# Performance work log

Hardware: AMD Instinct MI355X
Metric: run time of the kernel (lower is better)

## Reference

```python
import jax, jax.numpy as jnp
import numpy as np

WS = 7            # window size
NH = 6            # num heads
HD = 32           # head dim
DISP = WS // 2    # cyclic shift displacement (shifted=True)
SCALE = HD ** -0.5


def _create_mask(ws, d, upper_lower, left_right):
    m = np.zeros((ws * ws, ws * ws), np.float32)
    if upper_lower:
        m[-d * ws:, :-d * ws] = -np.inf
        m[:-d * ws, -d * ws:] = -np.inf
    if left_right:
        m = m.reshape(ws, ws, ws, ws)
        m[:, -d:, :, :-d] = -np.inf
        m[:, :-d, :, -d:] = -np.inf
        m = m.reshape(ws * ws, ws * ws)
    return m


def _relative_indices(ws):
    idx = np.array([[x, y] for x in range(ws) for y in range(ws)])
    return idx[None, :, :] - idx[:, None, :] + ws - 1  # (ws^2, ws^2, 2)


_REL = _relative_indices(WS)
_UL_MASK = _create_mask(WS, DISP, True, False)
_LR_MASK = _create_mask(WS, DISP, False, True)


def setup_inputs() -> dict:
    key = jax.random.key(0)
    ks = jax.random.split(key, 5)
    B, H, W, C = 32, 56, 56, 192
    inner = NH * HD
    return {
        "x": jax.random.normal(ks[0], (B, H, W, C), jnp.float32),
        "w_qkv": jax.random.normal(ks[1], (3 * inner, C), jnp.float32) * 0.02,
        "pos_embedding": jax.random.normal(ks[2], (2 * WS - 1, 2 * WS - 1), jnp.float32),
        "w_out": jax.random.normal(ks[3], (C, inner), jnp.float32) * 0.02,
        "b_out": jax.random.normal(ks[4], (C,), jnp.float32) * 0.02,
    }


def reference(x, w_qkv, pos_embedding, w_out, b_out):
    B, H, W, C = x.shape
    nwh, nww = H // WS, W // WS
    n = WS * WS
    nw = nwh * nww

    # cyclic shift
    x = jnp.roll(x, shift=(-DISP, -DISP), axis=(1, 2))

    qkv = x @ w_qkv.T  # (B,H,W,3*inner)

    def to_windows(t):
        # (B,H,W,inner) -> (B, NH, nw, n, HD)
        t = t.reshape(B, nwh, WS, nww, WS, NH, HD)
        t = t.transpose(0, 5, 1, 3, 2, 4, 6)
        return t.reshape(B, NH, nw, n, HD)

    q, k, v = map(to_windows, jnp.split(qkv, 3, axis=-1))

    dots = jnp.einsum('bhwid,bhwjd->bhwij', q, k) * SCALE

    # gathered relative-position bias
    bias = pos_embedding[_REL[:, :, 0], _REL[:, :, 1]]  # (n, n)
    dots = dots + bias

    # shift masks (static per-window additive mask)
    mask_full = np.zeros((nw, n, n), np.float32)
    mask_full[-nww:] += _UL_MASK
    mask_full[nww - 1::nww] += _LR_MASK
    dots = dots + jnp.asarray(mask_full)[None, None]

    attn = jax.nn.softmax(dots, axis=-1)
    out = jnp.einsum('bhwij,bhwjd->bhwid', attn, v)

    # windows back to image layout
    out = out.reshape(B, NH, nwh, nww, WS, WS, HD)
    out = out.transpose(0, 2, 4, 3, 5, 1, 6).reshape(B, H, W, NH * HD)

    out = out @ w_out.T + b_out
    return jnp.roll(out, shift=(DISP, DISP), axis=(1, 2))
```

## Files before the change

### kernel.cpp

```cpp
#include <hip/hip_runtime.h>
#include <hip/hip_bf16.h>

#define PIX 3136
#define MTOT 100352
#define SCALE 0.17677669529663687f

typedef __attribute__((ext_vector_type(8))) short bf16x8;
typedef __attribute__((ext_vector_type(4))) float f32x4;
typedef __attribute__((ext_vector_type(8))) unsigned short u16x8;

__device__ __forceinline__ unsigned short f2bf(float f) {
    __hip_bfloat16 h = __float2bfloat16(f);
    return *reinterpret_cast<unsigned short*>(&h);
}

__device__ __forceinline__ u16x8 packbf(float4 a, float4 b) {
    u16x8 r;
    r[0] = f2bf(a.x); r[1] = f2bf(a.y); r[2] = f2bf(a.z); r[3] = f2bf(a.w);
    r[4] = f2bf(b.x); r[5] = f2bf(b.y); r[6] = f2bf(b.z); r[7] = f2bf(b.w);
    return r;
}

__global__ __launch_bounds__(256) void qkv_mfma(
        const float* __restrict__ x, const float* __restrict__ wqkv,
        unsigned short* __restrict__ qo, unsigned short* __restrict__ ko,
        unsigned short* __restrict__ vo) {
    __shared__ __align__(16) unsigned char Al[128 * 384];
    __shared__ __align__(16) unsigned char Bl[64 * 384];
    const int tid = threadIdx.x;
    const int lane = tid & 63, wid = tid >> 6;
    const int G = lane >> 4, l16 = lane & 15;
    const int row0 = blockIdx.x * 128;

    {
        const int r = tid >> 1, half = tid & 1;
        const int gr = row0 + r;
        const int b = gr / PIX;
        const int rem = gr - b * PIX;
        const int w = rem / 49;
        const int i = rem - w * 49;
        const int yi = (i * 9363) >> 16;
        const int xi = i - yi * 7;
        int sh = (w >> 3) * 7 + yi + 3; if (sh >= 56) sh -= 56;
        int sw = (w & 7) * 7 + xi + 3; if (sw >= 56) sw -= 56;
        const float* src = x + ((size_t)(b * 56 + sh) * 56 + sw) * 192 + half * 96;
        const int swz = (r & 7) << 4;
#pragma unroll
        for (int c = 0; c < 12; c++) {
            float4 f0 = *(const float4*)(src + c * 8);
            float4 f1 = *(const float4*)(src + c * 8 + 4);
            const int off = half * 192 + c * 16;
            *(u16x8*)&Al[r * 384 + (off ^ swz)] = packbf(f0, f1);
        }
    }

    const int wr = wid >> 1, wc = wid & 1;
    f32x4 acc[4][2];
#pragma unroll
    for (int a = 0; a < 4; a++)
#pragma unroll
        for (int bb = 0; bb < 2; bb++) acc[a][bb] = (f32x4){0.f, 0.f, 0.f, 0.f};
    bf16x8 areg[4][6];

    for (int nt = 0; nt < 9; nt++) {
        __syncthreads();
        {
            const int rB = tid >> 2, q4 = tid & 3;
            const float* src = wqkv + (size_t)(nt * 64 + rB) * 192 + q4 * 48;
            const int swz = (rB & 7) << 4;
#pragma unroll
            for (int c = 0; c < 6; c++) {
                float4 f0 = *(const float4*)(src + c * 8);
                float4 f1 = *(const float4*)(src + c * 8 + 4);
                const int off = q4 * 96 + c * 16;
                *(u16x8*)&Bl[rB * 384 + (off ^ swz)] = packbf(f0, f1);
            }
        }
        __syncthreads();
        if (nt == 0) {
#pragma unroll
            for (int mi = 0; mi < 4; mi++) {
                const int rr = wr * 64 + mi * 16 + l16;
                const int swz = (rr & 7) << 4;
#pragma unroll
                for (int ks = 0; ks < 6; ks++)
                    areg[mi][ks] = *(const bf16x8*)&Al[rr * 384 + ((ks * 64 + G * 16) ^ swz)];
            }
        }
#pragma unroll
        for (int ks = 0; ks < 6; ks++) {
#pragma unroll
            for (int ni = 0; ni < 2; ni++) {
                const int rb = wc * 32 + ni * 16 + l16;
                bf16x8 bf = *(const bf16x8*)&Bl[rb * 384 + ((ks * 64 + G * 16) ^ ((rb & 7) << 4))];
#pragma unroll
                for (int mi = 0; mi < 4; mi++)
                    acc[mi][ni] = __builtin_amdgcn_mfma_f32_16x16x32_bf16(
                        areg[mi][ks], bf, acc[mi][ni], 0, 0, 0);
            }
        }
#pragma unroll
        for (int mi = 0; mi < 4; mi++) {
#pragma unroll
            for (int ni = 0; ni < 2; ni++) {
                const int nb = nt * 64 + wc * 32 + ni * 16;
                const int part = nb / 192;
                const int nn = nb - part * 192;
                const int head = nn >> 5;
                const int d = (nn & 31) + l16;
                unsigned short* dst = part == 0 ? qo : part == 1 ? ko : vo;
#pragma unroll
                for (int r = 0; r < 4; r++) {
                    const int rm = row0 + wr * 64 + mi * 16 + G * 4 + r;
                    const int b2 = rm / PIX;
                    const int rem2 = rm - b2 * PIX;
                    dst[((size_t)(b2 * 6 + head) * PIX + rem2) * 32 + d] = f2bf(acc[mi][ni][r]);
                    acc[mi][ni][r] = 0.f;
                }
            }
        }
    }
}

__global__ __launch_bounds__(256) void attn_mfma(
        const unsigned short* __restrict__ qg, const unsigned short* __restrict__ kg,
        const unsigned short* __restrict__ vg, const float* __restrict__ pe,
        unsigned short* __restrict__ ao) {
    __shared__ float pes[169];
    __shared__ __align__(16) unsigned char Pl[4][8192];
    __shared__ __align__(16) unsigned char Vl[4][4096];
    const int tid = threadIdx.x, lane = tid & 63, wid = tid >> 6;
    const int G = lane >> 4, l16 = lane & 15;
    if (tid < 169) pes[tid] = pe[tid];

    const int gw = blockIdx.x * 4 + wid;
    const int b = gw / 384;
    const int r384 = gw - b * 384;
    const int head = r384 >> 6;
    const int w = r384 & 63;
    const int wh = w >> 3, ww = w & 7;

#pragma unroll
    for (int z = 0; z < 4; z++)
        *(f32x4*)&Vl[wid][z * 1024 + lane * 16] = (f32x4){0.f, 0.f, 0.f, 0.f};

    const size_t base = ((size_t)(b * 6 + head) * PIX + w * 49) * 32;
    const unsigned short* qb = qg + base;
    const unsigned short* kb = kg + base;
    const unsigned short* vb = vg + base;

    for (int t = lane; t < 196; t += 64) {
        const int j = t >> 2, d0 = (t & 3) * 8;
        u16x8 vv = *(const u16x8*)(vb + j * 32 + d0);
#pragma unroll
        for (int e = 0; e < 8; e++) {
            const int d = d0 + e;
            *(unsigned short*)&Vl[wid][d * 128 + ((j * 2) ^ ((d & 7) << 4))] = vv[e];
        }
    }

    bf16x8 qf[4], kf[4];
    const bf16x8 zf = {0, 0, 0, 0, 0, 0, 0, 0};
#pragma unroll
    for (int mi = 0; mi < 4; mi++) {
        const int rr = mi * 16 + l16;
        qf[mi] = (rr < 49) ? *(const bf16x8*)(qb + rr * 32 + G * 8) : zf;
        kf[mi] = (rr < 49) ? *(const bf16x8*)(kb + rr * 32 + G * 8) : zf;
    }
    __syncthreads();

    const f32x4 zc = (f32x4){0.f, 0.f, 0.f, 0.f};
    f32x4 s[4][4];
#pragma unroll
    for (int mi = 0; mi < 4; mi++)
#pragma unroll
        for (int nj = 0; nj < 4; nj++)
            s[mi][nj] = __builtin_amdgcn_mfma_f32_16x16x32_bf16(qf[mi], kf[nj], zc, 0, 0, 0);

    const bool ulm = (wh == 7), lrm = (ww == 7);
    int jv[4], yj[4], xj[4];
#pragma unroll
    for (int nj = 0; nj < 4; nj++) {
        jv[nj] = nj * 16 + l16;
        yj[nj] = (jv[nj] * 9363) >> 16;
        xj[nj] = jv[nj] - yj[nj] * 7;
    }
    float rsc[4][4];
#pragma unroll
    for (int mi = 0; mi < 4; mi++) {
#pragma unroll
        for (int r = 0; r < 4; r++) {
            const int i = mi * 16 + G * 4 + r;
            const int yi = (i * 9363) >> 16;
            const int xi = i - yi * 7;
            float mx = -1e30f;
            float vals[4];
#pragma unroll
            for (int nj = 0; nj < 4; nj++) {
                const bool valid = (i < 49) && (jv[nj] < 49);
                const int bidx = valid ? ((yj[nj] - yi + 6) * 13 + (xj[nj] - xi + 6)) : 0;
                float val = s[mi][nj][r] * SCALE + pes[bidx];
                const bool dead = (!valid) || (ulm && ((yi >= 4) != (yj[nj] >= 4)))
                                           || (lrm && ((xi >= 4) != (xj[nj] >= 4)));
                vals[nj] = dead ? -1e30f : val;
                mx = fmaxf(mx, vals[nj]);
            }
#pragma unroll
            for (int m2 = 1; m2 < 16; m2 <<= 1) mx = fmaxf(mx, __shfl_xor(mx, m2));
            float sum = 0.f;
#pragma unroll
            for (int nj = 0; nj < 4; nj++) {
                const float e = __expf(vals[nj] - mx);
                s[mi][nj][r] = e;
                sum += e;
            }
#pragma unroll
            for (int m2 = 1; m2 < 16; m2 <<= 1) sum += __shfl_xor(sum, m2);
            rsc[mi][r] = 1.0f / sum;
        }
    }

#pragma unroll
    for (int mi = 0; mi < 4; mi++)
#pragma unroll
        for (int r = 0; r < 4; r++) {
            const int i = mi * 16 + G * 4 + r;
            const int swz = (i & 7) << 4;
#pragma unroll
            for (int nj = 0; nj < 4; nj++)
                *(unsigned short*)&Pl[wid][i * 128 + ((jv[nj] * 2) ^ swz)] = f2bf(s[mi][nj][r]);
        }

    f32x4 o[4][2];
#pragma unroll
    for (int mi = 0; mi < 4; mi++)
#pragma unroll
        for (int ni = 0; ni < 2; ni++) o[mi][ni] = zc;
#pragma unroll
    for (int ks = 0; ks < 2; ks++) {
        bf16x8 pa[4];
#pragma unroll
        for (int mi = 0; mi < 4; mi++) {
            const int i = mi * 16 + l16;
            pa[mi] = *(const bf16x8*)&Pl[wid][i * 128 + ((ks * 64 + G * 16) ^ ((i & 7) << 4))];
        }
#pragma unroll
        for (int ni = 0; ni < 2; ni++) {
            const int d = ni * 16 + l16;
            bf16x8 vf = *(const bf16x8*)&Vl[wid][d * 128 + ((ks * 64 + G * 16) ^ ((d & 7) << 4))];
#pragma unroll
            for (int mi = 0; mi < 4; mi++)
                o[mi][ni] = __builtin_amdgcn_mfma_f32_16x16x32_bf16(pa[mi], vf, o[mi][ni], 0, 0, 0);
        }
    }

#pragma unroll
    for (int mi = 0; mi < 4; mi++)
#pragma unroll
        for (int r = 0; r < 4; r++) {
            const int i = mi * 16 + G * 4 + r;
            if (i < 49) {
                const int yi = (i * 9363) >> 16;
                const int xi = i - yi * 7;
                int hf = wh * 7 + yi + 3; if (hf >= 56) hf -= 56;
                int wf = ww * 7 + xi + 3; if (wf >= 56) wf -= 56;
                const size_t orow = ((size_t)b * PIX + hf * 56 + wf) * 192 + head * 32;
                const float rs = rsc[mi][r];
#pragma unroll
                for (int ni = 0; ni < 2; ni++)
                    ao[orow + ni * 16 + l16] = f2bf(o[mi][ni][r] * rs);
            }
        }
}

__global__ __launch_bounds__(256) void proj_mfma(
        const unsigned short* __restrict__ ain, const float* __restrict__ wout,
        const float* __restrict__ bout, float* __restrict__ out) {
    __shared__ __align__(16) unsigned char Al[128 * 384];
    __shared__ __align__(16) unsigned char Bl[64 * 384];
    __shared__ float bls[192];
    const int tid = threadIdx.x;
    const int lane = tid & 63, wid = tid >> 6;
    const int G = lane >> 4, l16 = lane & 15;
    const int row0 = blockIdx.x * 128;
    if (tid < 192) bls[tid] = bout[tid];

    {
        const int r = tid >> 1, half = tid & 1;
        const unsigned short* src = ain + (size_t)(row0 + r) * 192 + half * 96;
        const int swz = (r & 7) << 4;
#pragma unroll
        for (int c = 0; c < 12; c++) {
            u16x8 v = *(const u16x8*)(src + c * 8);
            const int off = half * 192 + c * 16;
            *(u16x8*)&Al[r * 384 + (off ^ swz)] = v;
        }
    }

    const int wr = wid >> 1, wc = wid & 1;
    f32x4 acc[4][2];
#pragma unroll
    for (int a = 0; a < 4; a++)
#pragma unroll
        for (int bb = 0; bb < 2; bb++) acc[a][bb] = (f32x4){0.f, 0.f, 0.f, 0.f};
    bf16x8 areg[4][6];

    for (int nt = 0; nt < 3; nt++) {
        __syncthreads();
        {
            const int rB = tid >> 2, q4 = tid & 3;
            const float* src = wout + (size_t)(nt * 64 + rB) * 192 + q4 * 48;
            const int swz = (rB & 7) << 4;
#pragma unroll
            for (int c = 0; c < 6; c++) {
                float4 f0 = *(const float4*)(src + c * 8);
                float4 f1 = *(const float4*)(src + c * 8 + 4);
                const int off = q4 * 96 + c * 16;
                *(u16x8*)&Bl[rB * 384 + (off ^ swz)] = packbf(f0, f1);
            }
        }
        __syncthreads();
        if (nt == 0) {
#pragma unroll
            for (int mi = 0; mi < 4; mi++) {
                const int rr = wr * 64 + mi * 16 + l16;
                const int swz = (rr & 7) << 4;
#pragma unroll
                for (int ks = 0; ks < 6; ks++)
                    areg[mi][ks] = *(const bf16x8*)&Al[rr * 384 + ((ks * 64 + G * 16) ^ swz)];
            }
        }
#pragma unroll
        for (int ks = 0; ks < 6; ks++) {
#pragma unroll
            for (int ni = 0; ni < 2; ni++) {
                const int rb = wc * 32 + ni * 16 + l16;
                bf16x8 bf = *(const bf16x8*)&Bl[rb * 384 + ((ks * 64 + G * 16) ^ ((rb & 7) << 4))];
#pragma unroll
                for (int mi = 0; mi < 4; mi++)
                    acc[mi][ni] = __builtin_amdgcn_mfma_f32_16x16x32_bf16(
                        areg[mi][ks], bf, acc[mi][ni], 0, 0, 0);
            }
        }
#pragma unroll
        for (int mi = 0; mi < 4; mi++) {
#pragma unroll
            for (int ni = 0; ni < 2; ni++) {
                const int n = nt * 64 + wc * 32 + ni * 16 + l16;
                const float bias = bls[n];
#pragma unroll
                for (int r = 0; r < 4; r++) {
                    const int rm = row0 + wr * 64 + mi * 16 + G * 4 + r;
                    out[(size_t)rm * 192 + n] = acc[mi][ni][r] + bias;
                    acc[mi][ni][r] = 0.f;
                }
            }
        }
    }
}

extern "C" void kernel_launch(void* const* d_in, const int* in_sizes, int n_in,
                              void* d_out, int out_size, void* d_ws, size_t ws_size,
                              hipStream_t stream) {
    const float* x = (const float*)d_in[0];
    const float* wqkv = (const float*)d_in[1];
    const float* pe = (const float*)d_in[2];
    const float* wout = (const float*)d_in[3];
    const float* bout = (const float*)d_in[4];
    (void)in_sizes; (void)n_in; (void)out_size; (void)ws_size;

    const size_t per = (size_t)19267584;
    unsigned short* q = (unsigned short*)d_ws;
    unsigned short* k = q + per;
    unsigned short* v = k + per;
    unsigned short* ao = v + per;

    qkv_mfma<<<784, 256, 0, stream>>>(x, wqkv, q, k, v);
    attn_mfma<<<3072, 256, 0, stream>>>(q, k, v, pe, ao);
    proj_mfma<<<784, 256, 0, stream>>>(ao, wout, bout, (float*)d_out);
}
```

Measured before the change: 299.3 us.

## Fuse QKV projection, window attention, and output projection into one per-window kernel

Replaces the three kernels (QKV GEMM, attention, output GEMM) with a single kernel in which each block handles one shifted window and each of six waves handles one head. Q, K and V are computed straight into LDS, and the attention output is written back to LDS for the output projection. This removes the global bf16 round trips for q/k/v and the attention output. A small pre-kernel converts the weights to bf16 once per call, so each block reads bf16 weights directly from global/L2 instead of converting fp32 tiles in LDS. The trade-off is less weight reuse per block (64 rows padded from 49) and higher LDS and register pressure per block.

```diff
diff --git a/kernel.cpp b/kernel.cpp
--- a/kernel.cpp
+++ b/kernel.cpp
@@ -2,7 +2,6 @@
 #include <hip/hip_bf16.h>
 
 #define PIX 3136
-#define MTOT 100352
 #define SCALE 0.17677669529663687f
 
 typedef __attribute__((ext_vector_type(8))) short bf16x8;
@@ -13,7 +12,6 @@
     __hip_bfloat16 h = __float2bfloat16(f);
     return *reinterpret_cast<unsigned short*>(&h);
 }
-
 __device__ __forceinline__ u16x8 packbf(float4 a, float4 b) {
     u16x8 r;
     r[0] = f2bf(a.x); r[1] = f2bf(a.y); r[2] = f2bf(a.z); r[3] = f2bf(a.w);
@@ -21,155 +19,113 @@
     return r;
 }
 
-__global__ __launch_bounds__(256) void qkv_mfma(
-        const float* __restrict__ x, const float* __restrict__ wqkv,
-        unsigned short* __restrict__ qo, unsigned short* __restrict__ ko,
-        unsigned short* __restrict__ vo) {
-    __shared__ __align__(16) unsigned char Al[128 * 384];
-    __shared__ __align__(16) unsigned char Bl[64 * 384];
+__global__ __launch_bounds__(256) void convw(
+        const float* __restrict__ wqkv, const float* __restrict__ wout,
+        unsigned short* __restrict__ wqb, unsigned short* __restrict__ wob) {
+    const int t = blockIdx.x * 256 + threadIdx.x;
+    if (t < 13824) {
+        const float* s = wqkv + (size_t)t * 8;
+        float4 a = *(const float4*)s, b = *(const float4*)(s + 4);
+        *(u16x8*)(wqb + (size_t)t * 8) = packbf(a, b);
+    } else {
+        const int u = t - 13824;
+        const float* s = wout + (size_t)u * 8;
+        float4 a = *(const float4*)s, b = *(const float4*)(s + 4);
+        *(u16x8*)(wob + (size_t)u * 8) = packbf(a, b);
+    }
+}
+
+__global__ __launch_bounds__(384, 3) void fused_swin(
+        const float* __restrict__ x, const unsigned short* __restrict__ wq,
+        const unsigned short* __restrict__ wo, const float* __restrict__ pe,
+        const float* __restrict__ bout, float* __restrict__ out) {
+    __shared__ __align__(16) unsigned char Axl[64 * 384];
+    __shared__ __align__(16) unsigned char Scr[6][8704];
+    __shared__ float pes[169];
+    __shared__ float bls[192];
+
     const int tid = threadIdx.x;
-    const int lane = tid & 63, wid = tid >> 6;
+    const int lane = tid & 63, h = tid >> 6;
     const int G = lane >> 4, l16 = lane & 15;
-    const int row0 = blockIdx.x * 128;
+
+    const int blk = blockIdx.x;
+    const int b = blk >> 6, w = blk & 63;
+    const int wh = w >> 3, ww = w & 7;
+
+    if (tid < 169) pes[tid] = pe[tid];
+    else if (tid >= 192) bls[tid - 192] = bout[tid - 192];
 
     {
-        const int r = tid >> 1, half = tid & 1;
-        const int gr = row0 + r;
-        const int b = gr / PIX;
-        const int rem = gr - b * PIX;
-        const int w = rem / 49;
-        const int i = rem - w * 49;
-        const int yi = (i * 9363) >> 16;
-        const int xi = i - yi * 7;
-        int sh = (w >> 3) * 7 + yi + 3; if (sh >= 56) sh -= 56;
-        int sw = (w & 7) * 7 + xi + 3; if (sw >= 56) sw -= 56;
-        const float* src = x + ((size_t)(b * 56 + sh) * 56 + sw) * 192 + half * 96;
+        const int r = tid / 6, seg = tid % 6;
+        unsigned char* dst = Axl + r * 384;
         const int swz = (r & 7) << 4;
-#pragma unroll
-        for (int c = 0; c < 12; c++) {
-            float4 f0 = *(const float4*)(src + c * 8);
-            float4 f1 = *(const float4*)(src + c * 8 + 4);
-            const int off = half * 192 + c * 16;
-            *(u16x8*)&Al[r * 384 + (off ^ swz)] = packbf(f0, f1);
-        }
-    }
-
-    const int wr = wid >> 1, wc = wid & 1;
-    f32x4 acc[4][2];
-#pragma unroll
-    for (int a = 0; a < 4; a++)
-#pragma unroll
-        for (int bb = 0; bb < 2; bb++) acc[a][bb] = (f32x4){0.f, 0.f, 0.f, 0.f};
-    bf16x8 areg[4][6];
-
-    for (int nt = 0; nt < 9; nt++) {
-        __syncthreads();
-        {
-            const int rB = tid >> 2, q4 = tid & 3;
-            const float* src = wqkv + (size_t)(nt * 64 + rB) * 192 + q4 * 48;
-            const int swz = (rB & 7) << 4;
-#pragma unroll
-            for (int c = 0; c < 6; c++) {
+        if (r < 49) {
+            const int yi = r / 7, xi = r % 7;
+            int sh = wh * 7 + yi + 3; if (sh >= 56) sh -= 56;
+            int sw = ww * 7 + xi + 3; if (sw >= 56) sw -= 56;
+            const float* src = x + ((size_t)(b * 56 + sh) * 56 + sw) * 192 + seg * 32;
+#pragma unroll
+            for (int c = 0; c < 4; c++) {
                 float4 f0 = *(const float4*)(src + c * 8);
                 float4 f1 = *(const float4*)(src + c * 8 + 4);
-                const int off = q4 * 96 + c * 16;
-                *(u16x8*)&Bl[rB * 384 + (off ^ swz)] = packbf(f0, f1);
-            }
-        }
-        __syncthreads();
-        if (nt == 0) {
+                const int off = seg * 64 + c * 16;
+                *(u16x8*)&dst[off ^ swz] = packbf(f0, f1);
+            }
+        } else {
+            const u16x8 z = {0, 0, 0, 0, 0, 0, 0, 0};
+#pragma unroll
+            for (int c = 0; c < 4; c++) {
+                const int off = seg * 64 + c * 16;
+                *(u16x8*)&dst[off ^ swz] = z;
+            }
+        }
+    }
+    __syncthreads();
+
+    unsigned char* s0 = Scr[h];
+    unsigned char* sv = Scr[h] + 4608;
+
+    const f32x4 zc = (f32x4){0.f, 0.f, 0.f, 0.f};
+
+    bf16x8 qf[4], kf[4];
+#pragma unroll
+    for (int P = 0; P < 2; P++) {
+        f32x4 acc[4][2];
+#pragma unroll
+        for (int mi = 0; mi < 4; mi++) { acc[mi][0] = zc; acc[mi][1] = zc; }
+        const unsigned short* wbase = wq + (size_t)(P * 192 + h * 32) * 192;
+#pragma unroll
+        for (int ks = 0; ks < 6; ks++) {
+            bf16x8 b0 = *(const bf16x8*)(wbase + (size_t)l16 * 192 + ks * 32 + G * 8);
+            bf16x8 b1 = *(const bf16x8*)(wbase + (size_t)(16 + l16) * 192 + ks * 32 + G * 8);
 #pragma unroll
             for (int mi = 0; mi < 4; mi++) {
-                const int rr = wr * 64 + mi * 16 + l16;
-                const int swz = (rr & 7) << 4;
-#pragma unroll
-                for (int ks = 0; ks < 6; ks++)
-                    areg[mi][ks] = *(const bf16x8*)&Al[rr * 384 + ((ks * 64 + G * 16) ^ swz)];
-            }
-        }
-#pragma unroll
-        for (int ks = 0; ks < 6; ks++) {
-#pragma unroll
-            for (int ni = 0; ni < 2; ni++) {
-                const int rb = wc * 32 + ni * 16 + l16;
-                bf16x8 bf = *(const bf16x8*)&Bl[rb * 384 + ((ks * 64 + G * 16) ^ ((rb & 7) << 4))];
-#pragma unroll
-                for (int mi = 0; mi < 4; mi++)
-                    acc[mi][ni] = __builtin_amdgcn_mfma_f32_16x16x32_bf16(
-                        areg[mi][ks], bf, acc[mi][ni], 0, 0, 0);
-            }
-        }
+                const int row = mi * 16 + l16;
+                bf16x8 af = *(const bf16x8*)&Axl[row * 384 + ((ks * 64 + G * 16) ^ ((row & 7) << 4))];
+                acc[mi][0] = __builtin_amdgcn_mfma_f32_16x16x32_bf16(af, b0, acc[mi][0], 0, 0, 0);
+                acc[mi][1] = __builtin_amdgcn_mfma_f32_16x16x32_bf16(af, b1, acc[mi][1], 0, 0, 0);
+            }
+        }
+#pragma unroll
+        for (int mi = 0; mi < 4; mi++)
+#pragma unroll
+            for (int ni = 0; ni < 2; ni++)
+#pragma unroll
+                for (int r = 0; r < 4; r++) {
+                    const int row = mi * 16 + G * 4 + r;
+                    const int d = ni * 16 + l16;
+                    *(unsigned short*)&s0[row * 72 + d * 2] = f2bf(acc[mi][ni][r]);
+                }
 #pragma unroll
         for (int mi = 0; mi < 4; mi++) {
-#pragma unroll
-            for (int ni = 0; ni < 2; ni++) {
-                const int nb = nt * 64 + wc * 32 + ni * 16;
-                const int part = nb / 192;
-                const int nn = nb - part * 192;
-                const int head = nn >> 5;
-                const int d = (nn & 31) + l16;
-                unsigned short* dst = part == 0 ? qo : part == 1 ? ko : vo;
-#pragma unroll
-                for (int r = 0; r < 4; r++) {
-                    const int rm = row0 + wr * 64 + mi * 16 + G * 4 + r;
-                    const int b2 = rm / PIX;
-                    const int rem2 = rm - b2 * PIX;
-                    dst[((size_t)(b2 * 6 + head) * PIX + rem2) * 32 + d] = f2bf(acc[mi][ni][r]);
-                    acc[mi][ni][r] = 0.f;
-                }
-            }
-        }
-    }
-}
-
-__global__ __launch_bounds__(256) void attn_mfma(
-        const unsigned short* __restrict__ qg, const unsigned short* __restrict__ kg,
-        const unsigned short* __restrict__ vg, const float* __restrict__ pe,
-        unsigned short* __restrict__ ao) {
-    __shared__ float pes[169];
-    __shared__ __align__(16) unsigned char Pl[4][8192];
-    __shared__ __align__(16) unsigned char Vl[4][4096];
-    const int tid = threadIdx.x, lane = tid & 63, wid = tid >> 6;
-    const int G = lane >> 4, l16 = lane & 15;
-    if (tid < 169) pes[tid] = pe[tid];
-
-    const int gw = blockIdx.x * 4 + wid;
-    const int b = gw / 384;
-    const int r384 = gw - b * 384;
-    const int head = r384 >> 6;
-    const int w = r384 & 63;
-    const int wh = w >> 3, ww = w & 7;
-
-#pragma unroll
-    for (int z = 0; z < 4; z++)
-        *(f32x4*)&Vl[wid][z * 1024 + lane * 16] = (f32x4){0.f, 0.f, 0.f, 0.f};
-
-    const size_t base = ((size_t)(b * 6 + head) * PIX + w * 49) * 32;
-    const unsigned short* qb = qg + base;
-    const unsigned short* kb = kg + base;
-    const unsigned short* vb = vg + base;
-
-    for (int t = lane; t < 196; t += 64) {
-        const int j = t >> 2, d0 = (t & 3) * 8;
-        u16x8 vv = *(const u16x8*)(vb + j * 32 + d0);
-#pragma unroll
-        for (int e = 0; e < 8; e++) {
-            const int d = d0 + e;
-            *(unsigned short*)&Vl[wid][d * 128 + ((j * 2) ^ ((d & 7) << 4))] = vv[e];
-        }
-    }
-
-    bf16x8 qf[4], kf[4];
-    const bf16x8 zf = {0, 0, 0, 0, 0, 0, 0, 0};
-#pragma unroll
-    for (int mi = 0; mi < 4; mi++) {
-        const int rr = mi * 16 + l16;
-        qf[mi] = (rr < 49) ? *(const bf16x8*)(qb + rr * 32 + G * 8) : zf;
-        kf[mi] = (rr < 49) ? *(const bf16x8*)(kb + rr * 32 + G * 8) : zf;
-    }
-    __syncthreads();
-
-    const f32x4 zc = (f32x4){0.f, 0.f, 0.f, 0.f};
+            const int a = (mi * 16 + l16) * 72 + G * 16;
+            union { uint2 u[2]; bf16x8 f; } t;
+            t.u[0] = *(const uint2*)&s0[a];
+            t.u[1] = *(const uint2*)&s0[a + 8];
+            if (P == 0) qf[mi] = t.f; else kf[mi] = t.f;
+        }
+    }
+
     f32x4 s[4][4];
 #pragma unroll
     for (int mi = 0; mi < 4; mi++)
@@ -220,142 +176,118 @@
         }
     }
 
-#pragma unroll
-    for (int mi = 0; mi < 4; mi++)
-#pragma unroll
-        for (int r = 0; r < 4; r++) {
-            const int i = mi * 16 + G * 4 + r;
-            const int swz = (i & 7) << 4;
-#pragma unroll
-            for (int nj = 0; nj < 4; nj++)
-                *(unsigned short*)&Pl[wid][i * 128 + ((jv[nj] * 2) ^ swz)] = f2bf(s[mi][nj][r]);
-        }
+    {
+        f32x4 acc[4][2];
+#pragma unroll
+        for (int mi = 0; mi < 4; mi++) { acc[mi][0] = zc; acc[mi][1] = zc; }
+        const unsigned short* wbase = wq + (size_t)(384 + h * 32) * 192;
+#pragma unroll
+        for (int ks = 0; ks < 6; ks++) {
+            bf16x8 b0 = *(const bf16x8*)(wbase + (size_t)l16 * 192 + ks * 32 + G * 8);
+            bf16x8 b1 = *(const bf16x8*)(wbase + (size_t)(16 + l16) * 192 + ks * 32 + G * 8);
+#pragma unroll
+            for (int mi = 0; mi < 4; mi++) {
+                const int row = mi * 16 + l16;
+                bf16x8 af = *(const bf16x8*)&Axl[row * 384 + ((ks * 64 + G * 16) ^ ((row & 7) << 4))];
+                acc[mi][0] = __builtin_amdgcn_mfma_f32_16x16x32_bf16(af, b0, acc[mi][0], 0, 0, 0);
+                acc[mi][1] = __builtin_amdgcn_mfma_f32_16x16x32_bf16(af, b1, acc[mi][1], 0, 0, 0);
+            }
+        }
+#pragma unroll
+        for (int mi = 0; mi < 4; mi++)
+#pragma unroll
+            for (int ni = 0; ni < 2; ni++)
+#pragma unroll
+                for (int r = 0; r < 4; r++) {
+                    const int j = mi * 16 + G * 4 + r;
+                    const int d = ni * 16 + l16;
+                    *(unsigned short*)&sv[d * 128 + ((j * 2) ^ ((d & 7) << 4))] = f2bf(acc[mi][ni][r]);
+                }
+    }
 
     f32x4 o[4][2];
 #pragma unroll
-    for (int mi = 0; mi < 4; mi++)
-#pragma unroll
-        for (int ni = 0; ni < 2; ni++) o[mi][ni] = zc;
+    for (int mi = 0; mi < 4; mi++) { o[mi][0] = zc; o[mi][1] = zc; }
 #pragma unroll
     for (int ks = 0; ks < 2; ks++) {
+#pragma unroll
+        for (int mi = 0; mi < 4; mi++)
+#pragma unroll
+            for (int r = 0; r < 4; r++) {
+                const int row = mi * 16 + G * 4 + r;
+#pragma unroll
+                for (int njh = 0; njh < 2; njh++) {
+                    const int nj = ks * 2 + njh;
+                    *(unsigned short*)&s0[row * 72 + (njh * 16 + l16) * 2] = f2bf(s[mi][nj][r]);
+                }
+            }
         bf16x8 pa[4];
 #pragma unroll
         for (int mi = 0; mi < 4; mi++) {
-            const int i = mi * 16 + l16;
-            pa[mi] = *(const bf16x8*)&Pl[wid][i * 128 + ((ks * 64 + G * 16) ^ ((i & 7) << 4))];
+            const int a = (mi * 16 + l16) * 72 + G * 16;
+            union { uint2 u[2]; bf16x8 f; } t;
+            t.u[0] = *(const uint2*)&s0[a];
+            t.u[1] = *(const uint2*)&s0[a + 8];
+            pa[mi] = t.f;
         }
 #pragma unroll
         for (int ni = 0; ni < 2; ni++) {
             const int d = ni * 16 + l16;
-            bf16x8 vf = *(const bf16x8*)&Vl[wid][d * 128 + ((ks * 64 + G * 16) ^ ((d & 7) << 4))];
+            bf16x8 vf = *(const bf16x8*)&sv[d * 128 + ((ks * 64 + G * 16) ^ ((d & 7) << 4))];
 #pragma unroll
             for (int mi = 0; mi < 4; mi++)
                 o[mi][ni] = __builtin_amdgcn_mfma_f32_16x16x32_bf16(pa[mi], vf, o[mi][ni], 0, 0, 0);
         }
     }
 
+    __syncthreads();
 #pragma unroll
     for (int mi = 0; mi < 4; mi++)
 #pragma unroll
-        for (int r = 0; r < 4; r++) {
-            const int i = mi * 16 + G * 4 + r;
-            if (i < 49) {
-                const int yi = (i * 9363) >> 16;
-                const int xi = i - yi * 7;
-                int hf = wh * 7 + yi + 3; if (hf >= 56) hf -= 56;
-                int wf = ww * 7 + xi + 3; if (wf >= 56) wf -= 56;
-                const size_t orow = ((size_t)b * PIX + hf * 56 + wf) * 192 + head * 32;
-                const float rs = rsc[mi][r];
-#pragma unroll
-                for (int ni = 0; ni < 2; ni++)
-                    ao[orow + ni * 16 + l16] = f2bf(o[mi][ni][r] * rs);
-            }
-        }
-}
-
-__global__ __launch_bounds__(256) void proj_mfma(
-        const unsigned short* __restrict__ ain, const float* __restrict__ wout,
-        const float* __restrict__ bout, float* __restrict__ out) {
-    __shared__ __align__(16) unsigned char Al[128 * 384];
-    __shared__ __align__(16) unsigned char Bl[64 * 384];
-    __shared__ float bls[192];
-    const int tid = threadIdx.x;
-    const int lane = tid & 63, wid = tid >> 6;
-    const int G = lane >> 4, l16 = lane & 15;
-    const int row0 = blockIdx.x * 128;
-    if (tid < 192) bls[tid] = bout[tid];
+        for (int ni = 0; ni < 2; ni++)
+#pragma unroll
+            for (int r = 0; r < 4; r++) {
+                const int i = mi * 16 + G * 4 + r;
+                const int col = h * 32 + ni * 16 + l16;
+                *(unsigned short*)&Axl[i * 384 + ((col * 2) ^ ((i & 7) << 4))] =
+                    f2bf(o[mi][ni][r] * rsc[mi][r]);
+            }
+    __syncthreads();
 
     {
-        const int r = tid >> 1, half = tid & 1;
-        const unsigned short* src = ain + (size_t)(row0 + r) * 192 + half * 96;
-        const int swz = (r & 7) << 4;
-#pragma unroll
-        for (int c = 0; c < 12; c++) {
-            u16x8 v = *(const u16x8*)(src + c * 8);
-            const int off = half * 192 + c * 16;
-            *(u16x8*)&Al[r * 384 + (off ^ swz)] = v;
-        }
-    }
-
-    const int wr = wid >> 1, wc = wid & 1;
-    f32x4 acc[4][2];
-#pragma unroll
-    for (int a = 0; a < 4; a++)
-#pragma unroll
-        for (int bb = 0; bb < 2; bb++) acc[a][bb] = (f32x4){0.f, 0.f, 0.f, 0.f};
-    bf16x8 areg[4][6];
-
-    for (int nt = 0; nt < 3; nt++) {
-        __syncthreads();
-        {
-            const int rB = tid >> 2, q4 = tid & 3;
-            const float* src = wout + (size_t)(nt * 64 + rB) * 192 + q4 * 48;
-            const int swz = (rB & 7) << 4;
-#pragma unroll
-            for (int c = 0; c < 6; c++) {
-                float4 f0 = *(const float4*)(src + c * 8);
-                float4 f1 = *(const float4*)(src + c * 8 + 4);
-                const int off = q4 * 96 + c * 16;
-                *(u16x8*)&Bl[rB * 384 + (off ^ swz)] = packbf(f0, f1);
-            }
-        }
-        __syncthreads();
-        if (nt == 0) {
+        f32x4 acc[4][2];
+#pragma unroll
+        for (int mi = 0; mi < 4; mi++) { acc[mi][0] = zc; acc[mi][1] = zc; }
+        const unsigned short* wbase = wo + (size_t)(h * 32) * 192;
+#pragma unroll
+        for (int ks = 0; ks < 6; ks++) {
+            bf16x8 b0 = *(const bf16x8*)(wbase + (size_t)l16 * 192 + ks * 32 + G * 8);
+            bf16x8 b1 = *(const bf16x8*)(wbase + (size_t)(16 + l16) * 192 + ks * 32 + G * 8);
 #pragma unroll
             for (int mi = 0; mi < 4; mi++) {
-                const int rr = wr * 64 + mi * 16 + l16;
-                const int swz = (rr & 7) << 4;
-#pragma unroll
-                for (int ks = 0; ks < 6; ks++)
-                    areg[mi][ks] = *(const bf16x8*)&Al[rr * 384 + ((ks * 64 + G * 16) ^ swz)];
-            }
-        }
-#pragma unroll
-        for (int ks = 0; ks < 6; ks++) {
-#pragma unroll
-            for (int ni = 0; ni < 2; ni++) {
-                const int rb = wc * 32 + ni * 16 + l16;
-                bf16x8 bf = *(const bf16x8*)&Bl[rb * 384 + ((ks * 64 + G * 16) ^ ((rb & 7) << 4))];
-#pragma unroll
-                for (int mi = 0; mi < 4; mi++)
-                    acc[mi][ni] = __builtin_amdgcn_mfma_f32_16x16x32_bf16(
-                        areg[mi][ks], bf, acc[mi][ni], 0, 0, 0);
-            }
-        }
-#pragma unroll
-        for (int mi = 0; mi < 4; mi++) {
-#pragma unroll
-            for (int ni = 0; ni < 2; ni++) {
-                const int n = nt * 64 + wc * 32 + ni * 16 + l16;
-                const float bias = bls[n];
-#pragma unroll
-                for (int r = 0; r < 4; r++) {
-                    const int rm = row0 + wr * 64 + mi * 16 + G * 4 + r;
-                    out[(size_t)rm * 192 + n] = acc[mi][ni][r] + bias;
-                    acc[mi][ni][r] = 0.f;
+                const int row = mi * 16 + l16;
+                bf16x8 af = *(const bf16x8*)&Axl[row * 384 + ((ks * 64 + G * 16) ^ ((row & 7) << 4))];
+                acc[mi][0] = __builtin_amdgcn_mfma_f32_16x16x32_bf16(af, b0, acc[mi][0], 0, 0, 0);
+                acc[mi][1] = __builtin_amdgcn_mfma_f32_16x16x32_bf16(af, b1, acc[mi][1], 0, 0, 0);
+            }
+        }
+        const float bia0 = bls[h * 32 + l16];
+        const float bia1 = bls[h * 32 + 16 + l16];
+#pragma unroll
+        for (int mi = 0; mi < 4; mi++)
+#pragma unroll
+            for (int r = 0; r < 4; r++) {
+                const int i = mi * 16 + G * 4 + r;
+                if (i < 49) {
+                    const int yi = (i * 9363) >> 16;
+                    const int xi = i - yi * 7;
+                    int hf = wh * 7 + yi + 3; if (hf >= 56) hf -= 56;
+                    int wf = ww * 7 + xi + 3; if (wf >= 56) wf -= 56;
+                    float* orow = out + ((size_t)(b * PIX) + hf * 56 + wf) * 192 + h * 32;
+                    orow[l16] = acc[mi][0][r] + bia0;
+                    orow[16 + l16] = acc[mi][1][r] + bia1;
                 }
             }
-        }
     }
 }
 
@@ -369,13 +301,9 @@
     const float* bout = (const float*)d_in[4];
     (void)in_sizes; (void)n_in; (void)out_size; (void)ws_size;
 
-    const size_t per = (size_t)19267584;
-    unsigned short* q = (unsigned short*)d_ws;
-    unsigned short* k = q + per;
-    unsigned short* v = k + per;
-    unsigned short* ao = v + per;
-
-    qkv_mfma<<<784, 256, 0, stream>>>(x, wqkv, q, k, v);
-    attn_mfma<<<3072, 256, 0, stream>>>(q, k, v, pe, ao);
-    proj_mfma<<<784, 256, 0, stream>>>(ao, wout, bout, (float*)d_out);
-}
+    unsigned short* wqb = (unsigned short*)d_ws;
+    unsigned short* wob = wqb + 110592;
+
+    convw<<<72, 256, 0, stream>>>(wqkv, wout, wqb, wob);
+    fused_swin<<<2048, 384, 0, stream>>>(x, wqb, wob, pe, bout, (float*)d_out);
+}
```

New measurement: 283.5 us. 1.06x faster.
